# Kernel tuning notes

Hardware: AMD Instinct MI355X
Metric: run time of the kernel (lower is better)

## Reference

```python
import jax, jax.numpy as jnp
import numpy as np

VOCAB, D = 100000, 128
B, V, S = 1024, 20, 30
N_CLASS = 20
H0, H1 = 256, 128  # hidden_dims


def setup_inputs() -> dict:
    key = jax.random.key(0)
    ks = jax.random.split(key, 10)
    diag_idx = jax.random.randint(ks[0], (B, V, S), 0, VOCAB, dtype=jnp.int32)
    proc_idx = jax.random.randint(ks[1], (B, V, S), 0, VOCAB, dtype=jnp.int32)
    embedding = jax.random.normal(ks[2], (VOCAB, D), dtype=jnp.float32)
    # fc0: (2D -> H0), fc1: (H0 -> H1), fc2: (H1 -> n_class); torch Linear layout [out,in]
    W0 = jax.random.normal(ks[3], (H0, 2 * D), dtype=jnp.float32) * (1.0 / np.sqrt(2 * D))
    b0 = jnp.zeros((H0,), dtype=jnp.float32)
    W1 = jax.random.normal(ks[4], (H1, H0), dtype=jnp.float32) * (1.0 / np.sqrt(H0))
    b1 = jnp.zeros((H1,), dtype=jnp.float32)
    W2 = jax.random.normal(ks[5], (N_CLASS, H1), dtype=jnp.float32) * (1.0 / np.sqrt(H1))
    b2 = jnp.zeros((N_CLASS,), dtype=jnp.float32)
    return {"diag_idx": diag_idx, "proc_idx": proc_idx, "embedding": embedding,
            "W0": W0, "b0": b0, "W1": W1, "b1": b1, "W2": W2, "b2": b2}


def _pool(embedding, idx):
    # gather [B,V,S,D], mean over set dim S, sum over visit dim V -> [B,D]
    e = embedding[idx]
    return e.mean(axis=2).sum(axis=1)


def reference(diag_idx, proc_idx, embedding, W0, b0, W1, b1, W2, b2):
    d = _pool(embedding, diag_idx)            # [B, D]
    p = _pool(embedding, proc_idx)            # [B, D]
    x = jnp.concatenate([d, p], axis=-1)      # [B, 2D]
    out = x @ W0.T + b0                        # fc_layers[0]
    out = jax.nn.relu(out) @ W1.T + b1         # relu applied before each subsequent layer
    out = jax.nn.relu(out) @ W2.T + b2
    return out                                  # [B, n_class]
```

## Files before the change

kernel.cpp:

```cpp
#include <hip/hip_runtime.h>

#define BATCH 1024
#define VS 600
#define D 128
#define H0 256
#define H1 128
#define NCLASS 20
#define NB 32
#define PASSES 4
#define CAP 48
#define SPB 4


__global__ __launch_bounds__(256) void bucket_kernel(
    const int* __restrict__ diag_idx, const int* __restrict__ proc_idx,
    unsigned short* __restrict__ lists, int* __restrict__ counts)
{
    __shared__ int cnt[2 * NB];
    const int s = blockIdx.x, tid = threadIdx.x;
    if (tid < 2 * NB) cnt[tid] = 0;
    __syncthreads();

    const int* dsrc = diag_idx + s * VS;
    const int* psrc = proc_idx + s * VS;
    for (int i = tid; i < VS; i += 256) {
        const int r = dsrc[i];
        const int b = r & (NB - 1);
        const int pos = atomicAdd(&cnt[b], 1);
        if (pos < CAP) lists[((s * 2 + 0) * NB + b) * CAP + pos] = (unsigned short)(r >> 5);
        const int r2 = psrc[i];
        const int b2 = r2 & (NB - 1);
        const int pos2 = atomicAdd(&cnt[NB + b2], 1);
        if (pos2 < CAP) lists[((s * 2 + 1) * NB + b2) * CAP + pos2] = (unsigned short)(r2 >> 5);
    }
    __syncthreads();
    if (tid < 2 * NB) counts[s * 2 * NB + tid] = min(cnt[tid], CAP);
}

__global__ __launch_bounds__(256) void gather_partial_kernel(
    const unsigned short* __restrict__ lists, const int* __restrict__ counts,
    const float* __restrict__ emb, float* __restrict__ part, const int p)
{
    __shared__ unsigned short lq[2 * CAP];
    __shared__ int c2[2];
    __shared__ __attribute__((aligned(16))) float red[8][D];

    const int bid = blockIdx.x;
    const int x   = bid & 7;
    const int s   = bid >> 3;
    const int tid = threadIdx.x;
    const int b   = p * 8 + x;

    if (tid < 2) c2[tid] = counts[s * 2 * NB + tid * NB + b];
    if (tid < CAP)           lq[tid] = lists[((s * 2 + 0) * NB + b) * CAP + tid];
    else if (tid < 2 * CAP)  lq[tid] = lists[((s * 2 + 1) * NB + b) * CAP + (tid - CAP)];
    __syncthreads();

    const int grp = tid >> 5, lane = tid & 31;
    const int pool = grp >> 2, sub = grp & 3;
    const int cnt = c2[pool];
    const unsigned short* lp = lq + pool * CAP;
    float4 acc = make_float4(0.f, 0.f, 0.f, 0.f);
    for (int i = sub; i < cnt; i += 4) {
        const int row = ((int)lp[i] << 5) | b;
        const float4 e = ((const float4*)(emb + row * D))[lane];
        acc.x += e.x; acc.y += e.y; acc.z += e.z; acc.w += e.w;
    }
    ((float4*)red[grp])[lane] = acc;
    __syncthreads();

    {
        const int pl = tid >> 7, d = tid & 127;
        const float v = (red[pl*4+0][d] + red[pl*4+1][d] + red[pl*4+2][d] + red[pl*4+3][d])
                        * (1.0f / 30.0f);
        const int idx = (x * BATCH + s) * (2 * D) + tid;
        if (p == 0) part[idx] = v;
        else        part[idx] += v;
    }
}

__global__ __launch_bounds__(512) void mlp_kernel(
    const float* __restrict__ part,
    const float* __restrict__ W0, const float* __restrict__ b0,
    const float* __restrict__ W1, const float* __restrict__ b1,
    const float* __restrict__ W2, const float* __restrict__ b2,
    float* __restrict__ out)
{
    __shared__ __attribute__((aligned(16))) float xs [SPB][2 * D];
    __shared__ __attribute__((aligned(16))) float h0s[SPB][H0];
    __shared__ __attribute__((aligned(16))) float h1s[SPB][H1];

    const int s0 = blockIdx.x * SPB, tid = threadIdx.x;

    #pragma unroll
    for (int t = tid; t < SPB * 2 * D; t += 512) {
        const int j = t >> 8, d = t & 255;
        float v = 0.f;
        #pragma unroll
        for (int xp = 0; xp < 8; ++xp)
            v += part[(xp * BATCH + s0 + j) * (2 * D) + d];
        xs[j][d] = v;
    }
    __syncthreads();

    {
        const int row = tid >> 1, half = tid & 1;
        const float4* wrow = (const float4*)(W0 + row * (2 * D) + half * D);
        const int xoff = half * (D / 4);
        float a[SPB];
        #pragma unroll
        for (int j = 0; j < SPB; ++j) a[j] = 0.f;
        #pragma unroll 4
        for (int k = 0; k < 32; ++k) {
            const float4 w = wrow[k];
            #pragma unroll
            for (int j = 0; j < SPB; ++j) {
                const float4 xx = ((const float4*)xs[j])[xoff + k];
                a[j] += w.x * xx.x + w.y * xx.y + w.z * xx.z + w.w * xx.w;
            }
        }
        #pragma unroll
        for (int j = 0; j < SPB; ++j) {
            a[j] += __shfl_xor(a[j], 1);
            if (!half) h0s[j][row] = fmaxf(a[j] + b0[row], 0.f);
        }
    }
    __syncthreads();

    {
        const int row = tid >> 2, q = tid & 3;
        const float4* wrow = (const float4*)(W1 + row * H0 + q * 64);
        const int hoff = q * 16;
        float a[SPB];
        #pragma unroll
        for (int j = 0; j < SPB; ++j) a[j] = 0.f;
        #pragma unroll 4
        for (int k = 0; k < 16; ++k) {
            const float4 w = wrow[k];
            #pragma unroll
            for (int j = 0; j < SPB; ++j) {
                const float4 hh = ((const float4*)h0s[j])[hoff + k];
                a[j] += w.x * hh.x + w.y * hh.y + w.z * hh.z + w.w * hh.w;
            }
        }
        #pragma unroll
        for (int j = 0; j < SPB; ++j) {
            a[j] += __shfl_xor(a[j], 1);
            a[j] += __shfl_xor(a[j], 2);
            if (!q) h1s[j][row] = fmaxf(a[j] + b1[row], 0.f);
        }
    }
    __syncthreads();

    if (tid < NCLASS * 16) {
        const int row = tid >> 4, q = (tid >> 2) & 3, j = tid & 3;
        const float4* wrow = (const float4*)(W2 + row * H1 + q * 32);
        const float4* hv   = (const float4*)(h1s[j] + q * 32);
        float a = 0.f;
        #pragma unroll
        for (int k = 0; k < 8; ++k) {
            const float4 w = wrow[k], hh = hv[k];
            a += w.x * hh.x + w.y * hh.y + w.z * hh.z + w.w * hh.w;
        }
        a += __shfl_xor(a, 4);
        a += __shfl_xor(a, 8);
        if (!q) out[(s0 + j) * NCLASS + row] = a + b2[row];
    }
}

extern "C" void kernel_launch(void* const* d_in, const int* in_sizes, int n_in,
                              void* d_out, int out_size, void* d_ws, size_t ws_size,
                              hipStream_t stream) {
    const int*   diag_idx = (const int*)d_in[0];
    const int*   proc_idx = (const int*)d_in[1];
    const float* emb      = (const float*)d_in[2];
    const float* W0       = (const float*)d_in[3];
    const float* b0       = (const float*)d_in[4];
    const float* W1       = (const float*)d_in[5];
    const float* b1       = (const float*)d_in[6];
    const float* W2       = (const float*)d_in[7];
    const float* b2       = (const float*)d_in[8];
    float* out = (float*)d_out;

    char* ws = (char*)d_ws;
    float*          part   = (float*)ws;
    unsigned short* lists  = (unsigned short*)(ws + 8*1024*1024);
    int*            counts = (int*)(ws + 14*1024*1024);

    bucket_kernel<<<BATCH, 256, 0, stream>>>(diag_idx, proc_idx, lists, counts);
    for (int p = 0; p < PASSES; ++p)
        gather_partial_kernel<<<8 * BATCH, 256, 0, stream>>>(lists, counts, emb, part, p);
    mlp_kernel<<<BATCH / SPB, 512, 0, stream>>>(part, W0, b0, W1, b1, W2, b2, out);
}
```

Baseline: 176.3 us.

## Fuse four gather passes into one launch covering all bucket phases

The four separate gather launches become one. Each block now loads the bucket lists and counts for all four phases and accumulates every phase's embedding rows in registers before writing its partial sum once. This removes three kernel launches and the read-modify-write of the partial buffer on passes after the first. In exchange, each launch no longer restricts itself to one quarter of the embedding table, so any cache locality the per-pass split gave up is lost.

Result: faster. 162.5 us (-7.8%).

```diff
diff --git a/kernel.cpp b/kernel.cpp
--- a/kernel.cpp
+++ b/kernel.cpp
@@ -7,7 +7,7 @@
 #define H1 128
 #define NCLASS 20
 #define NB 32
-#define PASSES 4
+#define PHASES 4
 #define CAP 48
 #define SPB 4
 
@@ -39,43 +39,50 @@
 
 __global__ __launch_bounds__(256) void gather_partial_kernel(
     const unsigned short* __restrict__ lists, const int* __restrict__ counts,
-    const float* __restrict__ emb, float* __restrict__ part, const int p)
+    const float* __restrict__ emb, float* __restrict__ part)
 {
-    __shared__ unsigned short lq[2 * CAP];
-    __shared__ int c2[2];
+    __shared__ unsigned short lq[2 * PHASES * CAP];
+    __shared__ int c2[2 * PHASES];
     __shared__ __attribute__((aligned(16))) float red[8][D];
 
     const int bid = blockIdx.x;
     const int x   = bid & 7;
     const int s   = bid >> 3;
     const int tid = threadIdx.x;
-    const int b   = p * 8 + x;
-
-    if (tid < 2) c2[tid] = counts[s * 2 * NB + tid * NB + b];
-    if (tid < CAP)           lq[tid] = lists[((s * 2 + 0) * NB + b) * CAP + tid];
-    else if (tid < 2 * CAP)  lq[tid] = lists[((s * 2 + 1) * NB + b) * CAP + (tid - CAP)];
+
+    for (int t = tid; t < 2 * PHASES * CAP; t += 256) {
+        const int pl = t / (PHASES * CAP);
+        const int p  = (t / CAP) & (PHASES - 1);
+        const int j  = t % CAP;
+        lq[t] = lists[((s * 2 + pl) * NB + p * 8 + x) * CAP + j];
+    }
+    if (tid < 2 * PHASES) {
+        const int pl = tid >> 2, p = tid & 3;
+        c2[tid] = counts[s * 2 * NB + pl * NB + p * 8 + x];
+    }
     __syncthreads();
 
     const int grp = tid >> 5, lane = tid & 31;
     const int pool = grp >> 2, sub = grp & 3;
-    const int cnt = c2[pool];
-    const unsigned short* lp = lq + pool * CAP;
     float4 acc = make_float4(0.f, 0.f, 0.f, 0.f);
-    for (int i = sub; i < cnt; i += 4) {
-        const int row = ((int)lp[i] << 5) | b;
-        const float4 e = ((const float4*)(emb + row * D))[lane];
-        acc.x += e.x; acc.y += e.y; acc.z += e.z; acc.w += e.w;
+    #pragma unroll
+    for (int p = 0; p < PHASES; ++p) {
+        const int cnt = c2[pool * PHASES + p];
+        const unsigned short* lp = lq + (pool * PHASES + p) * CAP;
+        const int base = p * 8 + x;
+        for (int i = sub; i < cnt; i += 4) {
+            const int row = ((int)lp[i] << 5) | base;
+            const float4 e = ((const float4*)(emb + row * D))[lane];
+            acc.x += e.x; acc.y += e.y; acc.z += e.z; acc.w += e.w;
+        }
     }
     ((float4*)red[grp])[lane] = acc;
     __syncthreads();
 
     {
         const int pl = tid >> 7, d = tid & 127;
-        const float v = (red[pl*4+0][d] + red[pl*4+1][d] + red[pl*4+2][d] + red[pl*4+3][d])
-                        * (1.0f / 30.0f);
-        const int idx = (x * BATCH + s) * (2 * D) + tid;
-        if (p == 0) part[idx] = v;
-        else        part[idx] += v;
+        const float v = red[pl*4+0][d] + red[pl*4+1][d] + red[pl*4+2][d] + red[pl*4+3][d];
+        part[(x * BATCH + s) * (2 * D) + tid] = v * (1.0f / 30.0f);
     }
 }
 
@@ -188,7 +195,6 @@
     int*            counts = (int*)(ws + 14*1024*1024);
 
     bucket_kernel<<<BATCH, 256, 0, stream>>>(diag_idx, proc_idx, lists, counts);
-    for (int p = 0; p < PASSES; ++p)
-        gather_partial_kernel<<<8 * BATCH, 256, 0, stream>>>(lists, counts, emb, part, p);
+    gather_partial_kernel<<<8 * BATCH, 256, 0, stream>>>(lists, counts, emb, part);
     mlp_kernel<<<BATCH / SPB, 512, 0, stream>>>(part, W0, b0, W1, b1, W2, b2, out);
 }
```
